# Kernel optimization log

Measured on AMD Instinct MI355X. Metric: run time of the kernel, lower is better.

Reference implementation:

```python
import jax, jax.numpy as jnp
import numpy as np

B, N, D2, S = 64, 4096, 128, 512  # b, n, 2*d, size_s


def setup_inputs() -> dict:
    key = jax.random.key(0)
    k1, k2, k3, k4 = jax.random.split(key, 4)
    s_past = jax.random.randint(k1, (B, N), 0, S)
    yq = jax.random.normal(k2, (B, 1, D2), dtype=jnp.float32)
    y_past = jax.random.normal(k3, (B, N, D2), dtype=jnp.float32)
    w_mat = jax.random.normal(k4, (D2, D2), dtype=jnp.float32)
    return {"s_past": s_past, "yq": yq, "y_past": y_past, "w_mat": w_mat, "size_s": S}


def reference(s_past, yq, y_past, w_mat, size_s):
    # attn_logits[b,n] = yq[b,0,:] @ w_mat @ y_past[b,n,:]
    attn_logits = jnp.einsum('bqd,de,bne->bn', yq, w_mat, y_past)
    attn = jax.nn.softmax(attn_logits, axis=-1)  # (b, n)
    b, n = s_past.shape
    # post_est[b, s] = sum_n attn[b, n] * [s_past[b, n] == s]
    # fused scatter-add instead of materializing one-hot (b, n, S)
    flat_ids = (s_past + size_s * jnp.arange(b, dtype=s_past.dtype)[:, None]).reshape(-1)
    post_est = jax.ops.segment_sum(attn.reshape(-1), flat_ids,
                                   num_segments=b * size_s).reshape(b, size_s)
    return post_est
```

## Files before the change

### kernel.cpp

```cpp
#include <hip/hip_runtime.h>
#include <math.h>

#define BB 64
#define NN 4096
#define DD 128
#define SS 512
#define CHUNKS 16
#define ROWS_PER_BLOCK 256

__global__ void compute_q_kernel(const float* __restrict__ yq,
                                 const float* __restrict__ w,
                                 float* __restrict__ q) {
    int b = blockIdx.x;
    int e = threadIdx.x;
    __shared__ float syq[DD];
    syq[e] = yq[b * DD + e];
    __syncthreads();
    float acc = 0.f;
#pragma unroll
    for (int d = 0; d < DD; ++d) acc = fmaf(syq[d], w[d * DD + e], acc);
    q[b * DD + e] = acc;
}

__global__ void logits_kernel(const float* __restrict__ y_past,
                              const float* __restrict__ q,
                              float* __restrict__ logits,
                              float* __restrict__ pmax) {
    int b = blockIdx.x;
    int lane = threadIdx.x & 63;
    int wave = threadIdx.x >> 6;
    int n_base = blockIdx.y * ROWS_PER_BLOCK + wave * 64;

    float2 qv = ((const float2*)(q + b * DD))[lane];
    const float2* yp = (const float2*)(y_past + (size_t)b * NN * DD);

    float lmax = -1e30f;
    for (int i = 0; i < 64; ++i) {
        int n = n_base + i;
        float2 yv = yp[(size_t)n * 64 + lane];
        float p = fmaf(qv.x, yv.x, qv.y * yv.y);
#pragma unroll
        for (int off = 32; off > 0; off >>= 1) p += __shfl_xor(p, off, 64);
        if (lane == 0) logits[b * NN + n] = p;
        lmax = fmaxf(lmax, p);
    }

    __shared__ float smax[4];
    if (lane == 0) smax[wave] = lmax;
    __syncthreads();
    if (threadIdx.x == 0) {
        float m = fmaxf(fmaxf(smax[0], smax[1]), fmaxf(smax[2], smax[3]));
        pmax[b * CHUNKS + blockIdx.y] = m;
    }
}

__global__ void softmax_scatter_kernel(float* __restrict__ logits,
                                       const float* __restrict__ pmax,
                                       const int* __restrict__ s_past,
                                       float* __restrict__ out) {
    int b = blockIdx.x;
    int tid = threadIdx.x;
    __shared__ float bins[SS];
    __shared__ float red[8];
    __shared__ float s_m, s_inv;

    bins[tid] = 0.f;
    if (tid == 0) {
        float m = -1e30f;
        for (int c = 0; c < CHUNKS; ++c) m = fmaxf(m, pmax[b * CHUNKS + c]);
        s_m = m;
    }
    __syncthreads();

    float m = s_m;
    float lsum = 0.f;
#pragma unroll
    for (int k = 0; k < 8; ++k) {
        int n = tid + k * SS;
        float e = expf(logits[b * NN + n] - m);
        logits[b * NN + n] = e;
        lsum += e;
    }
#pragma unroll
    for (int off = 32; off > 0; off >>= 1) lsum += __shfl_xor(lsum, off, 64);
    int lane = tid & 63, wave = tid >> 6;
    if (lane == 0) red[wave] = lsum;
    __syncthreads();
    if (tid == 0) {
        float s = 0.f;
        for (int w2 = 0; w2 < 8; ++w2) s += red[w2];
        s_inv = 1.0f / s;
    }
    __syncthreads();

    float inv = s_inv;
#pragma unroll
    for (int k = 0; k < 8; ++k) {
        int n = tid + k * SS;
        float a = logits[b * NN + n] * inv;
        atomicAdd(&bins[s_past[b * NN + n]], a);
    }
    __syncthreads();
    out[b * SS + tid] = bins[tid];
}

extern "C" void kernel_launch(void* const* d_in, const int* in_sizes, int n_in,
                              void* d_out, int out_size, void* d_ws, size_t ws_size,
                              hipStream_t stream) {
    const int*   s_past = (const int*)d_in[0];
    const float* yq     = (const float*)d_in[1];
    const float* y_past = (const float*)d_in[2];
    const float* w_mat  = (const float*)d_in[3];

    float* ws     = (float*)d_ws;
    float* q      = ws;
    float* logits = q + BB * DD;
    float* pmax   = logits + BB * NN;
    float* out    = (float*)d_out;

    compute_q_kernel<<<BB, DD, 0, stream>>>(yq, w_mat, q);
    logits_kernel<<<dim3(BB, CHUNKS), 256, 0, stream>>>(y_past, q, logits, pmax);
    softmax_scatter_kernel<<<BB, SS, 0, stream>>>(logits, pmax, s_past, out);
}
```

Before: 230.3 us.

## Stage y_past tiles in LDS and fuse partial softmax sums into logits kernel

The logits kernel now loads y_past in float4 tiles into padded shared memory and computes each row's dot product with 4 threads per row, replacing one 64-wide shuffle reduction per row. It also computes per-chunk max and exp-sum, which gives an online-softmax combine. The scatter kernel then skips the separate exp/sum pass and the logits rewrite, and uses 1024 threads with vectorized loads and fast __expf. The extra LDS staging and syncs add overhead, and the fast exp slightly changes precision.

```diff
diff --git a/kernel.cpp b/kernel.cpp
--- a/kernel.cpp
+++ b/kernel.cpp
@@ -6,7 +6,8 @@
 #define DD 128
 #define SS 512
 #define CHUNKS 16
-#define ROWS_PER_BLOCK 256
+#define ROWS_PER_CHUNK 256
+#define SUBT 4
 
 __global__ void compute_q_kernel(const float* __restrict__ yq,
                                  const float* __restrict__ w,
@@ -22,86 +23,116 @@
     q[b * DD + e] = acc;
 }
 
-__global__ void logits_kernel(const float* __restrict__ y_past,
-                              const float* __restrict__ q,
-                              float* __restrict__ logits,
-                              float* __restrict__ pmax) {
-    int b = blockIdx.x;
-    int lane = threadIdx.x & 63;
-    int wave = threadIdx.x >> 6;
-    int n_base = blockIdx.y * ROWS_PER_BLOCK + wave * 64;
+__global__ __launch_bounds__(256) void logits_kernel(
+    const float* __restrict__ y_past, const float* __restrict__ q,
+    float* __restrict__ logits, float* __restrict__ pmax,
+    float* __restrict__ psum) {
+    int b = blockIdx.x, chunk = blockIdx.y;
+    int t = threadIdx.x;
 
-    float2 qv = ((const float2*)(q + b * DD))[lane];
-    const float2* yp = (const float2*)(y_past + (size_t)b * NN * DD);
+    __shared__ float4 ytile[64 * 33];
+    __shared__ float4 qsh4[32];
+    __shared__ float wred[8];
 
-    float lmax = -1e30f;
-    for (int i = 0; i < 64; ++i) {
-        int n = n_base + i;
-        float2 yv = yp[(size_t)n * 64 + lane];
-        float p = fmaf(qv.x, yv.x, qv.y * yv.y);
+    if (t < 32) qsh4[t] = ((const float4*)(q + b * DD))[t];
+    __syncthreads();
+
+    int j = t & 3;
+    int r = t >> 2;
+    float4 qreg[8];
 #pragma unroll
-        for (int off = 32; off > 0; off >>= 1) p += __shfl_xor(p, off, 64);
-        if (lane == 0) logits[b * NN + n] = p;
-        lmax = fmaxf(lmax, p);
+    for (int k = 0; k < 8; ++k) qreg[k] = qsh4[j * 8 + k];
+
+    const float4* gp =
+        (const float4*)y_past + ((size_t)b * NN + (size_t)chunk * ROWS_PER_CHUNK) * 32;
+
+    float pv[SUBT];
+#pragma unroll
+    for (int s = 0; s < SUBT; ++s) {
+#pragma unroll
+        for (int k = 0; k < 8; ++k) {
+            int idx = t + k * 256;
+            int rr = idx >> 5, cc = idx & 31;
+            ytile[rr * 33 + cc] = gp[s * 2048 + idx];
+        }
+        __syncthreads();
+
+        float4 acc = {0.f, 0.f, 0.f, 0.f};
+#pragma unroll
+        for (int k = 0; k < 8; ++k) {
+            float4 yv = ytile[r * 33 + j * 8 + k];
+            acc.x = fmaf(qreg[k].x, yv.x, acc.x);
+            acc.y = fmaf(qreg[k].y, yv.y, acc.y);
+            acc.z = fmaf(qreg[k].z, yv.z, acc.z);
+            acc.w = fmaf(qreg[k].w, yv.w, acc.w);
+        }
+        float p = (acc.x + acc.y) + (acc.z + acc.w);
+        p += __shfl_xor(p, 1, 64);
+        p += __shfl_xor(p, 2, 64);
+        if (j == 0)
+            logits[(size_t)b * NN + chunk * ROWS_PER_CHUNK + s * 64 + r] = p;
+        pv[s] = p;
+        __syncthreads();
     }
 
-    __shared__ float smax[4];
-    if (lane == 0) smax[wave] = lmax;
+    float m = fmaxf(fmaxf(pv[0], pv[1]), fmaxf(pv[2], pv[3]));
+#pragma unroll
+    for (int off = 32; off > 0; off >>= 1) m = fmaxf(m, __shfl_xor(m, off, 64));
+    int wave = t >> 6, lane = t & 63;
+    if (lane == 0) wred[wave] = m;
     __syncthreads();
-    if (threadIdx.x == 0) {
-        float m = fmaxf(fmaxf(smax[0], smax[1]), fmaxf(smax[2], smax[3]));
-        pmax[b * CHUNKS + blockIdx.y] = m;
+    m = fmaxf(fmaxf(wred[0], wred[1]), fmaxf(wred[2], wred[3]));
+
+    float ls = __expf(pv[0] - m) + __expf(pv[1] - m) + __expf(pv[2] - m) +
+               __expf(pv[3] - m);
+#pragma unroll
+    for (int off = 32; off > 0; off >>= 1) ls += __shfl_xor(ls, off, 64);
+    if (lane == 0) wred[4 + wave] = ls;
+    __syncthreads();
+    if (t == 0) {
+        pmax[b * CHUNKS + chunk] = m;
+        psum[b * CHUNKS + chunk] =
+            (wred[4] + wred[5] + wred[6] + wred[7]) * 0.25f;
     }
 }
 
-__global__ void softmax_scatter_kernel(float* __restrict__ logits,
-                                       const float* __restrict__ pmax,
-                                       const int* __restrict__ s_past,
-                                       float* __restrict__ out) {
+__global__ __launch_bounds__(1024) void scatter_kernel(
+    const float* __restrict__ logits, const float* __restrict__ pmax,
+    const float* __restrict__ psum, const int* __restrict__ s_past,
+    float* __restrict__ out) {
     int b = blockIdx.x;
-    int tid = threadIdx.x;
+    int t = threadIdx.x;
     __shared__ float bins[SS];
-    __shared__ float red[8];
-    __shared__ float s_m, s_inv;
+    __shared__ float cm[CHUNKS], cs[CHUNKS];
+    __shared__ float sM, sInv;
 
-    bins[tid] = 0.f;
-    if (tid == 0) {
-        float m = -1e30f;
-        for (int c = 0; c < CHUNKS; ++c) m = fmaxf(m, pmax[b * CHUNKS + c]);
-        s_m = m;
+    if (t < CHUNKS) {
+        cm[t] = pmax[b * CHUNKS + t];
+        cs[t] = psum[b * CHUNKS + t];
+    }
+    if (t < SS) bins[t] = 0.f;
+    __syncthreads();
+    if (t == 0) {
+        float M = cm[0];
+#pragma unroll
+        for (int i = 1; i < CHUNKS; ++i) M = fmaxf(M, cm[i]);
+        float S = 0.f;
+#pragma unroll
+        for (int i = 0; i < CHUNKS; ++i) S += cs[i] * __expf(cm[i] - M);
+        sM = M;
+        sInv = 1.f / S;
     }
     __syncthreads();
 
-    float m = s_m;
-    float lsum = 0.f;
-#pragma unroll
-    for (int k = 0; k < 8; ++k) {
-        int n = tid + k * SS;
-        float e = expf(logits[b * NN + n] - m);
-        logits[b * NN + n] = e;
-        lsum += e;
-    }
-#pragma unroll
-    for (int off = 32; off > 0; off >>= 1) lsum += __shfl_xor(lsum, off, 64);
-    int lane = tid & 63, wave = tid >> 6;
-    if (lane == 0) red[wave] = lsum;
+    float M = sM, inv = sInv;
+    float4 lg = ((const float4*)(logits + (size_t)b * NN))[t];
+    int4 sp = ((const int4*)(s_past + (size_t)b * NN))[t];
+    atomicAdd(&bins[sp.x], __expf(lg.x - M) * inv);
+    atomicAdd(&bins[sp.y], __expf(lg.y - M) * inv);
+    atomicAdd(&bins[sp.z], __expf(lg.z - M) * inv);
+    atomicAdd(&bins[sp.w], __expf(lg.w - M) * inv);
     __syncthreads();
-    if (tid == 0) {
-        float s = 0.f;
-        for (int w2 = 0; w2 < 8; ++w2) s += red[w2];
-        s_inv = 1.0f / s;
-    }
-    __syncthreads();
-
-    float inv = s_inv;
-#pragma unroll
-    for (int k = 0; k < 8; ++k) {
-        int n = tid + k * SS;
-        float a = logits[b * NN + n] * inv;
-        atomicAdd(&bins[s_past[b * NN + n]], a);
-    }
-    __syncthreads();
-    out[b * SS + tid] = bins[tid];
+    if (t < SS) out[b * SS + t] = bins[t];
 }
 
 extern "C" void kernel_launch(void* const* d_in, const int* in_sizes, int n_in,
@@ -116,9 +147,11 @@
     float* q      = ws;
     float* logits = q + BB * DD;
     float* pmax   = logits + BB * NN;
+    float* psum   = pmax + BB * CHUNKS;
     float* out    = (float*)d_out;
 
     compute_q_kernel<<<BB, DD, 0, stream>>>(yq, w_mat, q);
-    logits_kernel<<<dim3(BB, CHUNKS), 256, 0, stream>>>(y_past, q, logits, pmax);
-    softmax_scatter_kernel<<<BB, SS, 0, stream>>>(logits, pmax, s_past, out);
+    logits_kernel<<<dim3(BB, CHUNKS), 256, 0, stream>>>(y_past, q, logits,
+                                                        pmax, psum);
+    scatter_kernel<<<BB, 1024, 0, stream>>>(logits, pmax, psum, s_past, out);
 }
```

Measured after the change: 211.8 us. 1.09x faster.
